# Performance work log

Hardware: AMD Instinct MI355X
Metric: run time of the kernel (lower is better)

The kernel has to match this reference:

```python
import jax, jax.numpy as jnp
import numpy as np

N_Q_HEADS = 16
N_KV_HEADS = 4
HEAD_DIM = 64
GROUPS = N_Q_HEADS // N_KV_HEADS


def apply_rope(xq, xk, cos, sin):
    # xq: [B,S,Hq,D], xk: [B,S,Hkv,D]; cos/sin: [S, D/2]
    def rot(t):
        tr = t[..., 0::2]
        ti = t[..., 1::2]
        c = cos[None, :, None, :]
        s = sin[None, :, None, :]
        out_r = tr * c - ti * s
        out_i = tr * s + ti * c
        # interleave back: [..., D/2, 2] -> [..., D]
        return jnp.stack([out_r, out_i], axis=-1).reshape(t.shape)
    return rot(xq), rot(xk)


def setup_inputs() -> dict:
    key = jax.random.key(0)
    ks = jax.random.split(key, 8)
    B, S, DIM = 2, 2048, 1024
    x = jax.random.normal(ks[0], (B, S, DIM), jnp.float32)
    # RoPE frequencies (llama-style): theta_i = 10000^(-2i/D), angles = pos * theta
    inv_freq = 1.0 / (10000.0 ** (jnp.arange(0, HEAD_DIM, 2, dtype=jnp.float32) / HEAD_DIM))
    angles = jnp.arange(S, dtype=jnp.float32)[:, None] * inv_freq[None, :]  # [S, D/2]
    freqs_cos = jnp.cos(angles)
    freqs_sin = jnp.sin(angles)
    # additive causal mask [1,1,S,S]
    neg = jnp.float32(-1e9)
    mask = jnp.where(jnp.tril(jnp.ones((S, S), bool)), 0.0, neg)[None, None]
    scale = 0.02
    wq = jax.random.normal(ks[1], (DIM, N_Q_HEADS * HEAD_DIM), jnp.float32) * scale
    wk = jax.random.normal(ks[2], (DIM, N_KV_HEADS * HEAD_DIM), jnp.float32) * scale
    wv = jax.random.normal(ks[3], (DIM, N_KV_HEADS * HEAD_DIM), jnp.float32) * scale
    wo = jax.random.normal(ks[4], (DIM, DIM), jnp.float32) * scale
    return {"x": x, "start_pos": 0, "freqs_cos": freqs_cos, "freqs_sin": freqs_sin,
            "mask": mask, "wq": wq, "wk": wk, "wv": wv, "wo": wo}


def reference(x, start_pos, freqs_cos, freqs_sin, mask, wq, wk, wv, wo):
    B, S, DIM = x.shape
    xq = (x @ wq).reshape(B, S, N_Q_HEADS, HEAD_DIM)
    xk = (x @ wk).reshape(B, S, N_KV_HEADS, HEAD_DIM)
    xv = (x @ wv).reshape(B, S, N_KV_HEADS, HEAD_DIM)
    xq, xk = apply_rope(xq, xk, freqs_cos, freqs_sin)
    # seq_len > 1: prefill path, no KV-cache read. repeat_kv: expand kv heads by GROUPS.
    keys = jnp.repeat(xk, GROUPS, axis=2)    # [B,S,Hq,D]
    values = jnp.repeat(xv, GROUPS, axis=2)
    q = xq.transpose(0, 2, 1, 3)             # [B,H,S,D]
    k = keys.transpose(0, 2, 1, 3)
    v = values.transpose(0, 2, 1, 3)
    scores = jnp.einsum('bhqd,bhkd->bhqk', q, k) / jnp.sqrt(jnp.float32(HEAD_DIM))
    scores = scores + mask
    probs = jax.nn.softmax(scores, axis=-1)
    attn = jnp.einsum('bhqk,bhkd->bhqd', probs, v)  # [B,H,S,D]
    attn = attn.transpose(0, 2, 1, 3).reshape(B, S, DIM)
    return attn @ wo
```

## Files before the change

kernel.cpp:

```cpp
#include <hip/hip_runtime.h>

typedef __bf16 bf16_t;
typedef __bf16 bf16x8 __attribute__((ext_vector_type(8)));
typedef __bf16 bf16x4 __attribute__((ext_vector_type(4)));
typedef float f32x4 __attribute__((ext_vector_type(4)));
typedef short short4v __attribute__((ext_vector_type(4)));

#if __has_builtin(__builtin_amdgcn_exp2f)
#define EXP2F __builtin_amdgcn_exp2f
#else
#define EXP2F exp2f
#endif

#define BATCH 2
#define SEQ   2048
#define DIM   1024
#define NQH   16
#define NKVH  4
#define HD    64
#define ROWS  (BATCH*SEQ)
#define QKVN  1536
#define QSCALE 0.1803368801111f

static __device__ __forceinline__ short4v as_s4(bf16x4 v) {
    union { bf16x4 b; short4v s; } u; u.b = v; return u.s;
}

static __device__ __forceinline__ void gld16(const bf16_t* g, bf16_t* l) {
    __builtin_amdgcn_global_load_lds((const __attribute__((address_space(1))) void*)g,
                                     (__attribute__((address_space(3))) void*)l,
                                     16, 0, 0);
}

__global__ __launch_bounds__(256) void cast_x_kernel(const float* __restrict__ x,
                                                     bf16_t* __restrict__ o) {
    size_t i = ((size_t)blockIdx.x * 256 + threadIdx.x) * 4;
    float4 v = *(const float4*)(x + i);
    bf16x4 r;
    r[0] = (bf16_t)v.x; r[1] = (bf16_t)v.y; r[2] = (bf16_t)v.z; r[3] = (bf16_t)v.w;
    *(bf16x4*)(o + i) = r;
}

__global__ __launch_bounds__(256) void transpose_w_all(const float* __restrict__ wq,
                                                       const float* __restrict__ wk,
                                                       const float* __restrict__ wv,
                                                       const float* __restrict__ wo,
                                                       bf16_t* __restrict__ WqkvT,
                                                       bf16_t* __restrict__ WoT) {
    int bid = blockIdx.x;
    const float* src; bf16_t* dst; int N, nt, kt2;
    if (bid < 256)      { src = wq; dst = WqkvT;                      N = 1024; int i = bid;       nt = i & 15; kt2 = i >> 4; }
    else if (bid < 320) { src = wk; dst = WqkvT + (size_t)1024*1024;  N = 256;  int i = bid - 256; nt = i & 3;  kt2 = i >> 2; }
    else if (bid < 384) { src = wv; dst = WqkvT + (size_t)1280*1024;  N = 256;  int i = bid - 320; nt = i & 3;  kt2 = i >> 2; }
    else                { src = wo; dst = WoT;                        N = 1024; int i = bid - 384; nt = i & 15; kt2 = i >> 4; }

    __shared__ float tile[64][65];
    int t = threadIdx.x;
    {
        int r = t >> 2, cb = (t & 3) * 16;
        const float* s = src + (size_t)(kt2 * 64 + r) * N + nt * 64 + cb;
#pragma unroll
        for (int j = 0; j < 16; j += 4) {
            float4 v = *(const float4*)(s + j);
            tile[r][cb + j + 0] = v.x; tile[r][cb + j + 1] = v.y;
            tile[r][cb + j + 2] = v.z; tile[r][cb + j + 3] = v.w;
        }
    }
    __syncthreads();
    {
        int n = t >> 2, kb = (t & 3) * 16;
        union { bf16_t h[16]; uint4 u[2]; } pk;
#pragma unroll
        for (int j = 0; j < 16; ++j) pk.h[j] = (bf16_t)tile[kb + j][n];
        bf16_t* d = dst + (size_t)(nt * 64 + n) * 1024 + kt2 * 64 + kb;
        ((uint4*)d)[0] = pk.u[0];
        ((uint4*)d)[1] = pk.u[1];
    }
}

__global__ __launch_bounds__(256, 3) void gemm_qkv_kernel(const bf16_t* __restrict__ A,
                                                          const bf16_t* __restrict__ Bt,
                                                          const float* __restrict__ fcos,
                                                          const float* __restrict__ fsin,
                                                          bf16_t* __restrict__ Qb,
                                                          bf16_t* __restrict__ Kb,
                                                          bf16_t* __restrict__ Vt) {
    const int K = 1024;
    __shared__ __align__(16) bf16_t As[64 * 64];
    __shared__ __align__(16) bf16_t Bs[128 * 64];
    int t = threadIdx.x;
    int w = t >> 6, L = t & 63, quad = L >> 4, l15 = L & 15;
    int wr = (w >> 1) * 32, wc = (w & 1) * 64;

    int xid = blockIdx.x;
    int sw = (xid & 7) * 96 + (xid >> 3);
    int bnb = sw % 12;
    int bm = (sw / 12) * 64, bn = bnb * 128;

    int srow = L >> 3;
    int schunk = (L & 7) ^ srow;
    const bf16_t* Ag = A  + (size_t)(bm + w * 16 + srow) * K + schunk * 8;
    const bf16_t* Bg = Bt + (size_t)(bn + w * 32 + srow) * K + schunk * 8;
    bf16_t* Al = As + w * 1024;
    bf16_t* Bl = Bs + w * 2048;

    int rs0 = quad ^ (l15 & 7);
    int rs1 = (4 + quad) ^ (l15 & 7);

    f32x4 acc[2][4] = {};

    for (int k0 = 0; k0 < K; k0 += 64) {
        __syncthreads();
        gld16(Ag + k0,                 Al);
        gld16(Ag + (size_t)8 * K + k0, Al + 512);
#pragma unroll
        for (int c = 0; c < 4; ++c)
            gld16(Bg + (size_t)(c * 8) * K + k0, Bl + c * 512);
        __syncthreads();

#pragma unroll
        for (int kk = 0; kk < 2; ++kk) {
            int rsl = kk ? rs1 : rs0;
            bf16x8 a[2], b[4];
#pragma unroll
            for (int i = 0; i < 2; ++i)
                a[i] = ((const bf16x8*)As)[(wr + 16 * i + l15) * 8 + rsl];
#pragma unroll
            for (int j = 0; j < 4; ++j)
                b[j] = ((const bf16x8*)Bs)[(wc + 16 * j + l15) * 8 + rsl];
#pragma unroll
            for (int i = 0; i < 2; ++i)
#pragma unroll
                for (int j = 0; j < 4; ++j)
                    acc[i][j] = __builtin_amdgcn_mfma_f32_16x16x32_bf16(a[i], b[j], acc[i][j], 0, 0, 0);
        }
    }

    int region = (bnb >= 10) ? 2 : (bnb >= 8) ? 1 : 0;
#pragma unroll
    for (int i = 0; i < 2; ++i) {
        int row0 = bm + wr + 16 * i + quad * 4;
        int b = row0 >> 11, s0 = row0 & 2047;
#pragma unroll
        for (int j = 0; j < 4; ++j) {
            int col = bn + wc + 16 * j + l15;
            if (region == 2) {
                int kvh = (col >> 6) - 20, d = col & 63;
                bf16x4 o;
#pragma unroll
                for (int r = 0; r < 4; ++r) o[r] = (bf16_t)acc[i][j][r];
                *(bf16x4*)(Vt + ((size_t)((b * NKVH + kvh) * HD + d)) * SEQ + s0) = o;
            } else {
                int d = col & 63, fi = d >> 1;
                int odd = col & 1;
#pragma unroll
                for (int r = 0; r < 4; ++r) {
                    int s = s0 + r;
                    float v = acc[i][j][r];
                    float p = __shfl_xor(v, 1);
                    float c = fcos[s * 32 + fi], sn = fsin[s * 32 + fi];
                    float o = odd ? (p * sn + v * c) : (v * c - p * sn);
                    if (region == 0) {
                        int h = col >> 6;
                        Qb[((size_t)((b * NQH + h) * SEQ + s)) * HD + d] = (bf16_t)(o * QSCALE);
                    } else {
                        int kvh = (col >> 6) - 16;
                        Kb[((size_t)((b * NKVH + kvh) * SEQ + s)) * HD + d] = (bf16_t)o;
                    }
                }
            }
        }
    }
}

__global__ __launch_bounds__(256, 2) void gemm_bt_kernel(const bf16_t* __restrict__ A,
                                                         const bf16_t* __restrict__ Bt,
                                                         float* __restrict__ C) {
    const int K = 1024, N = 1024;
    __shared__ __align__(16) bf16_t As[64 * 64];
    __shared__ __align__(16) bf16_t Bs[128 * 64];
    int t = threadIdx.x;
    int w = t >> 6, L = t & 63, quad = L >> 4, l15 = L & 15;
    int wr = (w >> 1) * 32, wc = (w & 1) * 64;

    int xid = blockIdx.x;
    int sw = (xid & 7) * 64 + (xid >> 3);
    int bm = (sw >> 3) * 64, bn = (sw & 7) * 128;

    int srow = L >> 3;
    int schunk = (L & 7) ^ srow;
    const bf16_t* Ag = A  + (size_t)(bm + w * 16 + srow) * K + schunk * 8;
    const bf16_t* Bg = Bt + (size_t)(bn + w * 32 + srow) * K + schunk * 8;
    bf16_t* Al = As + w * 1024;
    bf16_t* Bl = Bs + w * 2048;

    int rs0 = quad ^ (l15 & 7);
    int rs1 = (4 + quad) ^ (l15 & 7);

    f32x4 acc[2][4] = {};

    for (int k0 = 0; k0 < K; k0 += 64) {
        __syncthreads();
        gld16(Ag + k0,                 Al);
        gld16(Ag + (size_t)8 * K + k0, Al + 512);
#pragma unroll
        for (int c = 0; c < 4; ++c)
            gld16(Bg + (size_t)(c * 8) * K + k0, Bl + c * 512);
        __syncthreads();

#pragma unroll
        for (int kk = 0; kk < 2; ++kk) {
            int rsl = kk ? rs1 : rs0;
            bf16x8 a[2], b[4];
#pragma unroll
            for (int i = 0; i < 2; ++i)
                a[i] = ((const bf16x8*)As)[(wr + 16 * i + l15) * 8 + rsl];
#pragma unroll
            for (int j = 0; j < 4; ++j)
                b[j] = ((const bf16x8*)Bs)[(wc + 16 * j + l15) * 8 + rsl];
#pragma unroll
            for (int i = 0; i < 2; ++i)
#pragma unroll
                for (int j = 0; j < 4; ++j)
                    acc[i][j] = __builtin_amdgcn_mfma_f32_16x16x32_bf16(a[i], b[j], acc[i][j], 0, 0, 0);
        }
    }

#pragma unroll
    for (int i = 0; i < 2; ++i) {
        int row = bm + wr + 16 * i + quad * 4;
#pragma unroll
        for (int j = 0; j < 4; ++j) {
            int col = bn + wc + 16 * j + l15;
            float* cp = C + (size_t)row * N + col;
#pragma unroll
            for (int r = 0; r < 4; ++r)
                cp[(size_t)r * N] = acc[i][j][r];
        }
    }
}

__global__ __launch_bounds__(256, 2) void attn_kernel(const bf16_t* __restrict__ Qb,
                                                      const bf16_t* __restrict__ Kb,
                                                      const bf16_t* __restrict__ Vt,
                                                      bf16_t* __restrict__ Ob) {
    int id = blockIdx.x;
    int sw = (id & 7) * 64 + (id >> 3);
    int b  = sw >> 8;
    int kv = (sw >> 6) & 3;
    int h  = kv * 4 + ((sw >> 4) & 3);
    int p  = sw & 15;

    int t = threadIdx.x, w = t >> 6, lane = t & 63, quad = lane >> 4, l15 = lane & 15;

    __shared__ __align__(16) bf16_t Ks[2][128 * 64];
    __shared__ __align__(16) bf16_t Vs[2][64 * 128];

    const bf16_t* Qbase = Qb + ((size_t)(b * NQH + h)) * SEQ * HD;
    const bf16_t* Kbase = Kb + ((size_t)(b * NKVH + kv)) * SEQ * HD;
    const bf16_t* Vbase = Vt + ((size_t)(b * NKVH + kv)) * HD * SEQ;

    const bf16_t* kS0 = Kbase + (size_t)(t >> 3) * HD + (size_t)(((t & 7) ^ ((t >> 3) & 7)) * 8);
    const bf16_t* vS0 = Vbase + (size_t)(t >> 4) * SEQ + (size_t)(((t & 15) ^ ((t >> 4) & 7)) * 8);
    int ldso = w * 512;

#pragma unroll 1
    for (int ph = 0; ph < 2; ++ph) {
        int qt = ph ? (31 - p) : p;
        int wq = qt * 64 + 16 * w + l15;
        int ktmax = qt >> 1;

        bf16x8 aq[2];
#pragma unroll
        for (int ks = 0; ks < 2; ++ks)
            aq[ks] = *(const bf16x8*)(Qbase + (size_t)wq * HD + ks * 32 + quad * 8);

        f32x4 acc_o[4] = {};
        float rs = 0.f;

        __syncthreads();
#pragma unroll
        for (int j = 0; j < 4; ++j) {
            gld16(kS0 + (size_t)j * 32 * HD, Ks[0] + ldso + j * 2048);
            gld16(vS0 + (size_t)j * 16 * SEQ, Vs[0] + ldso + j * 2048);
        }

        int cur = 0;
        for (int kt = 0; kt <= ktmax; ++kt) {
            __syncthreads();
            if (kt < ktmax) {
                const bf16_t* kp = kS0 + (size_t)(kt + 1) * 128 * HD;
                const bf16_t* vp = vS0 + (size_t)(kt + 1) * 128;
                bf16_t* kd = Ks[cur ^ 1] + ldso;
                bf16_t* vd = Vs[cur ^ 1] + ldso;
#pragma unroll
                for (int j = 0; j < 4; ++j) {
                    gld16(kp + (size_t)j * 32 * HD, kd + j * 2048);
                    gld16(vp + (size_t)j * 16 * SEQ, vd + j * 2048);
                }
            }
            const bf16_t* KsC = Ks[cur];
            const bf16_t* VsC = Vs[cur];

            short4v bp[8];
            if (kt == ktmax) {
                int kb = kt * 128 + quad * 4;
#pragma unroll
                for (int x = 0; x < 8; ++x) {
                    int key = 16 * x + l15;
                    bf16x8 ak0 = ((const bf16x8*)KsC)[key * 8 + ((0 + quad) ^ (key & 7))];
                    bf16x8 ak1 = ((const bf16x8*)KsC)[key * 8 + ((4 + quad) ^ (key & 7))];
                    f32x4 z = {0.f, 0.f, 0.f, 0.f};
                    z = __builtin_amdgcn_mfma_f32_16x16x32_bf16(ak0, aq[0], z, 0, 0, 0);
                    z = __builtin_amdgcn_mfma_f32_16x16x32_bf16(ak1, aq[1], z, 0, 0, 0);
                    bf16x4 pb;
#pragma unroll
                    for (int r = 0; r < 4; ++r) {
                        float pv = (kb + 16 * x + r <= wq) ? EXP2F(z[r]) : 0.f;
                        rs += pv; pb[r] = (bf16_t)pv;
                    }
                    bp[x] = as_s4(pb);
                }
            } else {
#pragma unroll
                for (int x = 0; x < 8; ++x) {
                    int key = 16 * x + l15;
                    bf16x8 ak0 = ((const bf16x8*)KsC)[key * 8 + ((0 + quad) ^ (key & 7))];
                    bf16x8 ak1 = ((const bf16x8*)KsC)[key * 8 + ((4 + quad) ^ (key & 7))];
                    f32x4 z = {0.f, 0.f, 0.f, 0.f};
                    z = __builtin_amdgcn_mfma_f32_16x16x32_bf16(ak0, aq[0], z, 0, 0, 0);
                    z = __builtin_amdgcn_mfma_f32_16x16x32_bf16(ak1, aq[1], z, 0, 0, 0);
                    bf16x4 pb;
#pragma unroll
                    for (int r = 0; r < 4; ++r) {
                        float pv = EXP2F(z[r]);
                        rs += pv; pb[r] = (bf16_t)pv;
                    }
                    bp[x] = as_s4(pb);
                }
            }

            __builtin_amdgcn_s_setprio(1);
#pragma unroll
            for (int dt = 0; dt < 4; ++dt) {
                int d = 16 * dt + l15;
#pragma unroll
                for (int x = 0; x < 8; ++x) {
                    int pos = (2 * x + (quad >> 1)) ^ (d & 7);
                    bf16x4 av = *(const bf16x4*)(VsC + d * 128 + pos * 8 + (quad & 1) * 4);
                    acc_o[dt] = __builtin_amdgcn_mfma_f32_16x16x16bf16_1k(as_s4(av), bp[x], acc_o[dt], 0, 0, 0);
                }
            }
            __builtin_amdgcn_s_setprio(0);
            cur ^= 1;
        }

        rs += __shfl_xor(rs, 16);
        rs += __shfl_xor(rs, 32);
        float rinv = 1.0f / rs;
        bf16_t* obase = Ob + (size_t)(b * SEQ + wq) * DIM + h * HD;
#pragma unroll
        for (int dt = 0; dt < 4; ++dt) {
            bf16x4 o;
#pragma unroll
            for (int r = 0; r < 4; ++r) o[r] = (bf16_t)(acc_o[dt][r] * rinv);
            *(bf16x4*)(obase + 16 * dt + quad * 4) = o;
        }
    }
}

extern "C" void kernel_launch(void* const* d_in, const int* in_sizes, int n_in,
                              void* d_out, int out_size, void* d_ws, size_t ws_size,
                              hipStream_t stream) {
    const float* x    = (const float*)d_in[0];
    const float* fcos = (const float*)d_in[2];
    const float* fsin = (const float*)d_in[3];
    const float* wq   = (const float*)d_in[5];
    const float* wk   = (const float*)d_in[6];
    const float* wv   = (const float*)d_in[7];
    const float* wo   = (const float*)d_in[8];
    float* out = (float*)d_out;

    char* ws = (char*)d_ws;
    bf16_t* Xb    = (bf16_t*)(ws + 0);
    bf16_t* Attnb = Xb;
    bf16_t* WqkvT = (bf16_t*)(ws + 8388608);
    bf16_t* WoT   = (bf16_t*)(ws + 11534336);
    bf16_t* Qb    = (bf16_t*)(ws + 13631488);
    bf16_t* Kb    = (bf16_t*)(ws + 22020096);
    bf16_t* Vt    = (bf16_t*)(ws + 24117248);

    cast_x_kernel<<<ROWS * DIM / 1024, 256, 0, stream>>>(x, Xb);
    transpose_w_all<<<640, 256, 0, stream>>>(wq, wk, wv, wo, WqkvT, WoT);

    gemm_qkv_kernel<<<(QKVN / 128) * (ROWS / 64), 256, 0, stream>>>(Xb, WqkvT, fcos, fsin, Qb, Kb, Vt);

    attn_kernel<<<512, 256, 0, stream>>>(Qb, Kb, Vt, Attnb);

    gemm_bt_kernel<<<(DIM / 128) * (ROWS / 64), 256, 0, stream>>>(Attnb, WoT, out);
}
```

Before: 167.3 us.

## Double-buffer LDS tiles in GEMMs and merge input-cast and weight-transpose kernels

Both bf16 GEMM kernels (the QKV projection with RoPE epilogue and the output projection) now keep two LDS buffers. The next K-tile's global-to-LDS loads are issued before the MFMAs on the current tile, and the loop needs only one barrier per iteration instead of two. Separately, the x-to-bf16 cast and the weight transpose/cast are merged into a single prep launch to save one kernel launch. The cost is double the shared memory per block, which could lower occupancy. Overlap also depends on the compiler not inserting a full vmcnt wait before the LDS reads.

```diff
diff --git a/kernel.cpp b/kernel.cpp
--- a/kernel.cpp
+++ b/kernel.cpp
@@ -32,22 +32,24 @@
                                      16, 0, 0);
 }
 
-__global__ __launch_bounds__(256) void cast_x_kernel(const float* __restrict__ x,
-                                                     bf16_t* __restrict__ o) {
-    size_t i = ((size_t)blockIdx.x * 256 + threadIdx.x) * 4;
-    float4 v = *(const float4*)(x + i);
-    bf16x4 r;
-    r[0] = (bf16_t)v.x; r[1] = (bf16_t)v.y; r[2] = (bf16_t)v.z; r[3] = (bf16_t)v.w;
-    *(bf16x4*)(o + i) = r;
-}
-
-__global__ __launch_bounds__(256) void transpose_w_all(const float* __restrict__ wq,
-                                                       const float* __restrict__ wk,
-                                                       const float* __restrict__ wv,
-                                                       const float* __restrict__ wo,
-                                                       bf16_t* __restrict__ WqkvT,
-                                                       bf16_t* __restrict__ WoT) {
+__global__ __launch_bounds__(256) void prep_kernel(const float* __restrict__ x,
+                                                   const float* __restrict__ wq,
+                                                   const float* __restrict__ wk,
+                                                   const float* __restrict__ wv,
+                                                   const float* __restrict__ wo,
+                                                   bf16_t* __restrict__ Xb,
+                                                   bf16_t* __restrict__ WqkvT,
+                                                   bf16_t* __restrict__ WoT) {
     int bid = blockIdx.x;
+    int t = threadIdx.x;
+    if (bid >= 640) {
+        size_t i = ((size_t)(bid - 640) * 256 + t) * 4;
+        float4 v = *(const float4*)(x + i);
+        bf16x4 r;
+        r[0] = (bf16_t)v.x; r[1] = (bf16_t)v.y; r[2] = (bf16_t)v.z; r[3] = (bf16_t)v.w;
+        *(bf16x4*)(Xb + i) = r;
+        return;
+    }
     const float* src; bf16_t* dst; int N, nt, kt2;
     if (bid < 256)      { src = wq; dst = WqkvT;                      N = 1024; int i = bid;       nt = i & 15; kt2 = i >> 4; }
     else if (bid < 320) { src = wk; dst = WqkvT + (size_t)1024*1024;  N = 256;  int i = bid - 256; nt = i & 3;  kt2 = i >> 2; }
@@ -55,7 +57,6 @@
     else                { src = wo; dst = WoT;                        N = 1024; int i = bid - 384; nt = i & 15; kt2 = i >> 4; }
 
     __shared__ float tile[64][65];
-    int t = threadIdx.x;
     {
         int r = t >> 2, cb = (t & 3) * 16;
         const float* s = src + (size_t)(kt2 * 64 + r) * N + nt * 64 + cb;
@@ -86,8 +87,8 @@
                                                           bf16_t* __restrict__ Kb,
                                                           bf16_t* __restrict__ Vt) {
     const int K = 1024;
-    __shared__ __align__(16) bf16_t As[64 * 64];
-    __shared__ __align__(16) bf16_t Bs[128 * 64];
+    __shared__ __align__(16) bf16_t As[2][64 * 64];
+    __shared__ __align__(16) bf16_t Bs[2][128 * 64];
     int t = threadIdx.x;
     int w = t >> 6, L = t & 63, quad = L >> 4, l15 = L & 15;
     int wr = (w >> 1) * 32, wc = (w & 1) * 64;
@@ -101,22 +102,36 @@
     int schunk = (L & 7) ^ srow;
     const bf16_t* Ag = A  + (size_t)(bm + w * 16 + srow) * K + schunk * 8;
     const bf16_t* Bg = Bt + (size_t)(bn + w * 32 + srow) * K + schunk * 8;
-    bf16_t* Al = As + w * 1024;
-    bf16_t* Bl = Bs + w * 2048;
 
     int rs0 = quad ^ (l15 & 7);
     int rs1 = (4 + quad) ^ (l15 & 7);
 
     f32x4 acc[2][4] = {};
 
+    {
+        bf16_t* Al = As[0] + w * 1024;
+        bf16_t* Bl = Bs[0] + w * 2048;
+        gld16(Ag,                 Al);
+        gld16(Ag + (size_t)8 * K, Al + 512);
+#pragma unroll
+        for (int c = 0; c < 4; ++c)
+            gld16(Bg + (size_t)(c * 8) * K, Bl + c * 512);
+    }
+
+    int cur = 0;
     for (int k0 = 0; k0 < K; k0 += 64) {
         __syncthreads();
-        gld16(Ag + k0,                 Al);
-        gld16(Ag + (size_t)8 * K + k0, Al + 512);
-#pragma unroll
-        for (int c = 0; c < 4; ++c)
-            gld16(Bg + (size_t)(c * 8) * K + k0, Bl + c * 512);
-        __syncthreads();
+        if (k0 + 64 < K) {
+            bf16_t* Al = As[cur ^ 1] + w * 1024;
+            bf16_t* Bl = Bs[cur ^ 1] + w * 2048;
+            gld16(Ag + k0 + 64,                 Al);
+            gld16(Ag + (size_t)8 * K + k0 + 64, Al + 512);
+#pragma unroll
+            for (int c = 0; c < 4; ++c)
+                gld16(Bg + (size_t)(c * 8) * K + k0 + 64, Bl + c * 512);
+        }
+        const bf16_t* Asc = As[cur];
+        const bf16_t* Bsc = Bs[cur];
 
 #pragma unroll
         for (int kk = 0; kk < 2; ++kk) {
@@ -124,16 +139,17 @@
             bf16x8 a[2], b[4];
 #pragma unroll
             for (int i = 0; i < 2; ++i)
-                a[i] = ((const bf16x8*)As)[(wr + 16 * i + l15) * 8 + rsl];
+                a[i] = ((const bf16x8*)Asc)[(wr + 16 * i + l15) * 8 + rsl];
 #pragma unroll
             for (int j = 0; j < 4; ++j)
-                b[j] = ((const bf16x8*)Bs)[(wc + 16 * j + l15) * 8 + rsl];
+                b[j] = ((const bf16x8*)Bsc)[(wc + 16 * j + l15) * 8 + rsl];
 #pragma unroll
             for (int i = 0; i < 2; ++i)
 #pragma unroll
                 for (int j = 0; j < 4; ++j)
                     acc[i][j] = __builtin_amdgcn_mfma_f32_16x16x32_bf16(a[i], b[j], acc[i][j], 0, 0, 0);
         }
+        cur ^= 1;
     }
 
     int region = (bnb >= 10) ? 2 : (bnb >= 8) ? 1 : 0;
@@ -177,8 +193,8 @@
                                                          const bf16_t* __restrict__ Bt,
                                                          float* __restrict__ C) {
     const int K = 1024, N = 1024;
-    __shared__ __align__(16) bf16_t As[64 * 64];
-    __shared__ __align__(16) bf16_t Bs[128 * 64];
+    __shared__ __align__(16) bf16_t As[2][64 * 64];
+    __shared__ __align__(16) bf16_t Bs[2][128 * 64];
     int t = threadIdx.x;
     int w = t >> 6, L = t & 63, quad = L >> 4, l15 = L & 15;
     int wr = (w >> 1) * 32, wc = (w & 1) * 64;
@@ -191,22 +207,36 @@
     int schunk = (L & 7) ^ srow;
     const bf16_t* Ag = A  + (size_t)(bm + w * 16 + srow) * K + schunk * 8;
     const bf16_t* Bg = Bt + (size_t)(bn + w * 32 + srow) * K + schunk * 8;
-    bf16_t* Al = As + w * 1024;
-    bf16_t* Bl = Bs + w * 2048;
 
     int rs0 = quad ^ (l15 & 7);
     int rs1 = (4 + quad) ^ (l15 & 7);
 
     f32x4 acc[2][4] = {};
 
+    {
+        bf16_t* Al = As[0] + w * 1024;
+        bf16_t* Bl = Bs[0] + w * 2048;
+        gld16(Ag,                 Al);
+        gld16(Ag + (size_t)8 * K, Al + 512);
+#pragma unroll
+        for (int c = 0; c < 4; ++c)
+            gld16(Bg + (size_t)(c * 8) * K, Bl + c * 512);
+    }
+
+    int cur = 0;
     for (int k0 = 0; k0 < K; k0 += 64) {
         __syncthreads();
-        gld16(Ag + k0,                 Al);
-        gld16(Ag + (size_t)8 * K + k0, Al + 512);
-#pragma unroll
-        for (int c = 0; c < 4; ++c)
-            gld16(Bg + (size_t)(c * 8) * K + k0, Bl + c * 512);
-        __syncthreads();
+        if (k0 + 64 < K) {
+            bf16_t* Al = As[cur ^ 1] + w * 1024;
+            bf16_t* Bl = Bs[cur ^ 1] + w * 2048;
+            gld16(Ag + k0 + 64,                 Al);
+            gld16(Ag + (size_t)8 * K + k0 + 64, Al + 512);
+#pragma unroll
+            for (int c = 0; c < 4; ++c)
+                gld16(Bg + (size_t)(c * 8) * K + k0 + 64, Bl + c * 512);
+        }
+        const bf16_t* Asc = As[cur];
+        const bf16_t* Bsc = Bs[cur];
 
 #pragma unroll
         for (int kk = 0; kk < 2; ++kk) {
@@ -214,16 +244,17 @@
             bf16x8 a[2], b[4];
 #pragma unroll
             for (int i = 0; i < 2; ++i)
-                a[i] = ((const bf16x8*)As)[(wr + 16 * i + l15) * 8 + rsl];
+                a[i] = ((const bf16x8*)Asc)[(wr + 16 * i + l15) * 8 + rsl];
 #pragma unroll
             for (int j = 0; j < 4; ++j)
-                b[j] = ((const bf16x8*)Bs)[(wc + 16 * j + l15) * 8 + rsl];
+                b[j] = ((const bf16x8*)Bsc)[(wc + 16 * j + l15) * 8 + rsl];
 #pragma unroll
             for (int i = 0; i < 2; ++i)
 #pragma unroll
                 for (int j = 0; j < 4; ++j)
                     acc[i][j] = __builtin_amdgcn_mfma_f32_16x16x32_bf16(a[i], b[j], acc[i][j], 0, 0, 0);
         }
+        cur ^= 1;
     }
 
 #pragma unroll
@@ -390,8 +421,7 @@
     bf16_t* Kb    = (bf16_t*)(ws + 22020096);
     bf16_t* Vt    = (bf16_t*)(ws + 24117248);
 
-    cast_x_kernel<<<ROWS * DIM / 1024, 256, 0, stream>>>(x, Xb);
-    transpose_w_all<<<640, 256, 0, stream>>>(wq, wk, wv, wo, WqkvT, WoT);
+    prep_kernel<<<640 + ROWS * DIM / 1024, 256, 0, stream>>>(x, wq, wk, wv, wo, Xb, WqkvT, WoT);
 
     gemm_qkv_kernel<<<(QKVN / 128) * (ROWS / 64), 256, 0, stream>>>(Xb, WqkvT, fcos, fsin, Qb, Kb, Vt);
 
```

After: 174.5 us. 1.04x slower.
